# Kernel optimization log

Hardware: AMD Instinct MI355X
Metric: run time of the kernel (lower is better)

Reference implementation:

```python
import jax, jax.numpy as jnp
import numpy as np

D_MODEL = 1024
N_HEADS = 16
HEAD_DIM = D_MODEL // N_HEADS
D_C = 128
THETA = 10000.0


def rope_cos_sin(timestamps):
    # timestamps: (B, L) -> cos, sin: (B, L, HEAD_DIM)
    freqs = 1.0 / (THETA ** (jnp.arange(0, HEAD_DIM, 2, dtype=jnp.float32) / HEAD_DIM))
    t = timestamps[..., None] * freqs            # (B, L, HEAD_DIM//2)
    emb = jnp.concatenate([t, t], axis=-1)       # (B, L, HEAD_DIM)
    return jnp.cos(emb), jnp.sin(emb)


def rotate_half(x):
    x1, x2 = jnp.split(x, 2, axis=-1)
    return jnp.concatenate([-x2, x1], axis=-1)


def setup_inputs() -> dict:
    key = jax.random.key(0)
    ks = jax.random.split(key, 10)
    B, L = 2, 2048
    s = 0.02
    return {
        "query": jax.random.normal(ks[0], (B, L, D_MODEL), jnp.float32),
        "timestamps_q": jax.random.uniform(ks[1], (B, L), jnp.float32) * 365.0,
        "timestamps_kv": jax.random.uniform(ks[2], (B, L), jnp.float32) * 365.0,
        "w_kv_c": jax.random.normal(ks[3], (D_MODEL, D_C), jnp.float32) * s,
        "w_kc_up": jax.random.normal(ks[4], (D_C, D_MODEL), jnp.float32) * s,
        "w_vc_up": jax.random.normal(ks[5], (D_C, D_MODEL), jnp.float32) * s,
        "w_qr": jax.random.normal(ks[6], (D_MODEL, D_MODEL), jnp.float32) * s,
        "w_kr": jax.random.normal(ks[7], (D_MODEL, D_MODEL), jnp.float32) * s,
        "w_o": jax.random.normal(ks[8], (D_MODEL, D_MODEL), jnp.float32) * s,
    }


def reference(query, timestamps_q, timestamps_kv, w_kv_c, w_kc_up, w_vc_up, w_qr, w_kr, w_o):
    B, Lq, _ = query.shape
    key_value = query  # self-attention path (key_value defaults to query)
    Lk = key_value.shape[1]

    def heads(x, L):  # (B, L, D) -> (B, H, L, hd)
        return x.reshape(B, L, N_HEADS, HEAD_DIM).transpose(0, 2, 1, 3)

    c_kv = key_value @ w_kv_c                      # (B, Lk, d_c) low-rank KV
    k_c = heads(c_kv @ w_kc_up, Lk)
    v_c = heads(c_kv @ w_vc_up, Lk)
    q_r = heads(query @ w_qr, Lq)
    k_r = heads(key_value @ w_kr, Lk)

    cos_q, _ = rope_cos_sin(timestamps_q)
    cos_k, _ = rope_cos_sin(timestamps_kv)
    cos_q = cos_q[:, None]                          # (B, 1, Lq, hd)
    cos_k = cos_k[:, None]                          # (B, 1, Lk, hd)
    # Faithful to original (which passes cos_k in the `sin` slot):
    q_r = q_r * cos_q + rotate_half(q_r) * cos_k
    k_r = k_r * cos_q + rotate_half(k_r) * cos_k

    scale = HEAD_DIM ** -0.5
    qs = q_r * scale
    attn = jnp.einsum("bhqd,bhkd->bhqk", qs, k_c) + jnp.einsum("bhqd,bhkd->bhqk", qs, k_r)
    attn_weights = jax.nn.softmax(attn, axis=-1)
    out = jnp.einsum("bhqk,bhkd->bhqd", attn_weights, v_c)
    out = out.transpose(0, 2, 1, 3).reshape(B, Lq, D_MODEL)
    return out @ w_o
```

## Files before the change

kernel.cpp:

```cpp
#include <hip/hip_runtime.h>

typedef float          f32x4    __attribute__((ext_vector_type(4)));
typedef float          float8v  __attribute__((ext_vector_type(8)));
typedef unsigned short ushort8v __attribute__((ext_vector_type(8)));
typedef __bf16         bf16x8   __attribute__((ext_vector_type(8)));
typedef __bf16         bf16x4   __attribute__((ext_vector_type(4)));

__device__ __forceinline__ unsigned short f2b(float x) {
  union { __bf16 b; unsigned short u; } v;
  v.b = (__bf16)x;
  return v.u;
}
__device__ __forceinline__ float b2f(unsigned short h) {
  union { unsigned u; float f; } v; v.u = ((unsigned)h) << 16;
  return v.f;
}
__device__ __forceinline__ void lds_fence() {
  __builtin_amdgcn_wave_barrier();
  asm volatile("s_waitcnt lgkmcnt(0)" ::: "memory");
}

__device__ __forceinline__ void g2lds16(const unsigned short* g,
                                        unsigned short* l) {
  __builtin_amdgcn_global_load_lds(
      (const __attribute__((address_space(1))) unsigned int*)g,
      (__attribute__((address_space(3))) unsigned int*)l, 16, 0, 0);
}

__global__ void cvt_kernel(const float* __restrict__ src,
                           unsigned short* __restrict__ dst, int n8) {
  int i = blockIdx.x * 256 + threadIdx.x;
  if (i >= n8) return;
  float8v v = reinterpret_cast<const float8v*>(src)[i];
  ushort8v h;
#pragma unroll
  for (int j = 0; j < 8; ++j) h[j] = f2b(v[j]);
  reinterpret_cast<ushort8v*>(dst)[i] = h;
}

__global__ __launch_bounds__(256) void wtrans_kernel(
    const float* __restrict__ W, unsigned short* __restrict__ WT,
    int K, int N) {
  __shared__ unsigned short T[64 * 72];
  const int tid = threadIdx.x;
  const int n0 = blockIdx.x * 64, k0 = blockIdx.y * 64;
#pragma unroll
  for (int it = 0; it < 2; ++it) {
    int c = tid + it * 256;
    int r = c >> 3, cc = c & 7;
    float8v v = *reinterpret_cast<const float8v*>(
        &W[(size_t)(k0 + r) * N + n0 + cc * 8]);
    ushort8v h;
#pragma unroll
    for (int j = 0; j < 8; ++j) h[j] = f2b(v[j]);
    *reinterpret_cast<ushort8v*>(&T[r * 72 + cc * 8]) = h;
  }
  __syncthreads();
#pragma unroll
  for (int it = 0; it < 2; ++it) {
    int c = tid + it * 256;
    int n = c >> 3, kc = c & 7;
    ushort8v y;
#pragma unroll
    for (int j = 0; j < 8; ++j) y[j] = T[(kc * 8 + j) * 72 + n];
    *reinterpret_cast<ushort8v*>(&WT[(size_t)(n0 + n) * K + k0 + kc * 8]) = y;
  }
}

template <int TM, typename CT, bool ACC>
__global__ __launch_bounds__(256) void gemm_bt(
    const unsigned short* __restrict__ A, const unsigned short* __restrict__ Bt,
    CT* __restrict__ C, int M, int N, int K) {
  __shared__ unsigned short As[TM * 64];
  __shared__ unsigned short Bs[128 * 64];
  const int tid = threadIdx.x;
  const int m0 = blockIdx.y * TM, n0 = blockIdx.x * 128;
  const int wave = tid >> 6, lane = tid & 63;
  const int wm = (wave >> 1) * (TM / 2), wn = (wave & 1) * 64;
  const int l16 = lane & 15, quad = lane >> 4;
  constexpr int MI = TM / 32;

  f32x4 acc[MI][4];
#pragma unroll
  for (int i = 0; i < MI; ++i)
#pragma unroll
    for (int j = 0; j < 4; ++j)
#pragma unroll
      for (int r = 0; r < 4; ++r) acc[i][j][r] = 0.f;

  for (int k0 = 0; k0 < K; k0 += 64) {
    __syncthreads();
#pragma unroll
    for (int it = 0; it < TM * 8 / 256; ++it) {
      int c = it * 256 + tid;
      int m = c >> 3, kc = (c & 7) ^ (m & 7);
      g2lds16(&A[(size_t)(m0 + m) * K + k0 + kc * 8], &As[c * 8]);
    }
#pragma unroll
    for (int it = 0; it < 4; ++it) {
      int c = it * 256 + tid;
      int n = c >> 3, kc = (c & 7) ^ (n & 7);
      g2lds16(&Bt[(size_t)(n0 + n) * K + k0 + kc * 8], &Bs[c * 8]);
    }
    __syncthreads();

#pragma unroll
    for (int ks = 0; ks < 2; ++ks) {
      bf16x8 af[MI], bfr[4];
#pragma unroll
      for (int mi = 0; mi < MI; ++mi) {
        int m = wm + mi * 16 + l16;
        af[mi] = *reinterpret_cast<const bf16x8*>(
            &As[(m * 8 + ((ks * 4 + quad) ^ (m & 7))) * 8]);
      }
#pragma unroll
      for (int ni = 0; ni < 4; ++ni) {
        int n = wn + ni * 16 + l16;
        bfr[ni] = *reinterpret_cast<const bf16x8*>(
            &Bs[(n * 8 + ((ks * 4 + quad) ^ (n & 7))) * 8]);
      }
#pragma unroll
      for (int mi = 0; mi < MI; ++mi)
#pragma unroll
        for (int ni = 0; ni < 4; ++ni)
          acc[mi][ni] = __builtin_amdgcn_mfma_f32_16x16x32_bf16(
              af[mi], bfr[ni], acc[mi][ni], 0, 0, 0);
    }
  }

#pragma unroll
  for (int mi = 0; mi < MI; ++mi)
#pragma unroll
    for (int ni = 0; ni < 4; ++ni) {
      int row = m0 + wm + mi * 16 + quad * 4;
      int col = n0 + wn + ni * 16 + l16;
#pragma unroll
      for (int r = 0; r < 4; ++r) {
        size_t idx = (size_t)(row + r) * N + col;
        float val = acc[mi][ni][r];
        if constexpr (sizeof(CT) == 2) {
          if constexpr (ACC) val += b2f(C[idx]);
          C[idx] = f2b(val);
        } else {
          if constexpr (ACC) val += C[idx];
          C[idx] = val;
        }
      }
    }
}

__global__ __launch_bounds__(256) void gemm_fused3(
    const unsigned short* __restrict__ A, const unsigned short* __restrict__ Bt,
    unsigned short* __restrict__ Cq, unsigned short* __restrict__ Ck,
    unsigned short* __restrict__ Cc, int K) {
  __shared__ unsigned short As[1024 * 8];
  __shared__ unsigned short Bs[1024 * 8];
  const int tid = threadIdx.x;
  const int m0 = blockIdx.y * 128, n0 = blockIdx.x * 128;
  const int wave = tid >> 6, lane = tid & 63;
  const int wm = (wave >> 1) * 64, wn = (wave & 1) * 64;
  const int l16 = lane & 15, quad = lane >> 4;

  f32x4 acc[4][4];
#pragma unroll
  for (int i = 0; i < 4; ++i)
#pragma unroll
    for (int j = 0; j < 4; ++j)
#pragma unroll
      for (int r = 0; r < 4; ++r) acc[i][j][r] = 0.f;

  for (int k0 = 0; k0 < K; k0 += 64) {
    __syncthreads();
#pragma unroll
    for (int it = 0; it < 4; ++it) {
      int c = it * 256 + tid;
      int m = c >> 3, kc = (c & 7) ^ (m & 7);
      g2lds16(&A[(size_t)(m0 + m) * K + k0 + kc * 8], &As[c * 8]);
    }
#pragma unroll
    for (int it = 0; it < 4; ++it) {
      int c = it * 256 + tid;
      int n = c >> 3, kc = (c & 7) ^ (n & 7);
      g2lds16(&Bt[(size_t)(n0 + n) * K + k0 + kc * 8], &Bs[c * 8]);
    }
    __syncthreads();

#pragma unroll
    for (int ks = 0; ks < 2; ++ks) {
      bf16x8 af[4], bfr[4];
#pragma unroll
      for (int mi = 0; mi < 4; ++mi) {
        int m = wm + mi * 16 + l16;
        af[mi] = *reinterpret_cast<const bf16x8*>(
            &As[(m * 8 + ((ks * 4 + quad) ^ (m & 7))) * 8]);
      }
#pragma unroll
      for (int ni = 0; ni < 4; ++ni) {
        int n = wn + ni * 16 + l16;
        bfr[ni] = *reinterpret_cast<const bf16x8*>(
            &Bs[(n * 8 + ((ks * 4 + quad) ^ (n & 7))) * 8]);
      }
#pragma unroll
      for (int mi = 0; mi < 4; ++mi)
#pragma unroll
        for (int ni = 0; ni < 4; ++ni)
          acc[mi][ni] = __builtin_amdgcn_mfma_f32_16x16x32_bf16(
              af[mi], bfr[ni], acc[mi][ni], 0, 0, 0);
    }
  }

  unsigned short* dst;
  int w, cb;
  if (n0 < 1024)      { dst = Cq; w = 1024; cb = 0; }
  else if (n0 < 2048) { dst = Ck; w = 1024; cb = 1024; }
  else                { dst = Cc; w = 128;  cb = 2048; }
#pragma unroll
  for (int mi = 0; mi < 4; ++mi)
#pragma unroll
    for (int ni = 0; ni < 4; ++ni) {
      int row = m0 + wm + mi * 16 + quad * 4;
      int col = n0 - cb + wn + ni * 16 + l16;
#pragma unroll
      for (int r = 0; r < 4; ++r)
        dst[(size_t)(row + r) * w + col] = f2b(acc[mi][ni][r]);
    }
}

__global__ __launch_bounds__(256) void gemm_fused2(
    const unsigned short* __restrict__ A, const unsigned short* __restrict__ Bt,
    unsigned short* __restrict__ Ck, unsigned short* __restrict__ Cv, int K) {
  __shared__ unsigned short As[1024 * 8];
  __shared__ unsigned short Bs[1024 * 8];
  const int tid = threadIdx.x;
  const int m0 = blockIdx.y * 128, n0 = blockIdx.x * 128;
  const int wave = tid >> 6, lane = tid & 63;
  const int wm = (wave >> 1) * 64, wn = (wave & 1) * 64;
  const int l16 = lane & 15, quad = lane >> 4;

  f32x4 acc[4][4];
#pragma unroll
  for (int i = 0; i < 4; ++i)
#pragma unroll
    for (int j = 0; j < 4; ++j)
#pragma unroll
      for (int r = 0; r < 4; ++r) acc[i][j][r] = 0.f;

  for (int k0 = 0; k0 < K; k0 += 64) {
    __syncthreads();
#pragma unroll
    for (int it = 0; it < 4; ++it) {
      int c = it * 256 + tid;
      int m = c >> 3, kc = (c & 7) ^ (m & 7);
      g2lds16(&A[(size_t)(m0 + m) * K + k0 + kc * 8], &As[c * 8]);
    }
#pragma unroll
    for (int it = 0; it < 4; ++it) {
      int c = it * 256 + tid;
      int n = c >> 3, kc = (c & 7) ^ (n & 7);
      g2lds16(&Bt[(size_t)(n0 + n) * K + k0 + kc * 8], &Bs[c * 8]);
    }
    __syncthreads();

#pragma unroll
    for (int ks = 0; ks < 2; ++ks) {
      bf16x8 af[4], bfr[4];
#pragma unroll
      for (int mi = 0; mi < 4; ++mi) {
        int m = wm + mi * 16 + l16;
        af[mi] = *reinterpret_cast<const bf16x8*>(
            &As[(m * 8 + ((ks * 4 + quad) ^ (m & 7))) * 8]);
      }
#pragma unroll
      for (int ni = 0; ni < 4; ++ni) {
        int n = wn + ni * 16 + l16;
        bfr[ni] = *reinterpret_cast<const bf16x8*>(
            &Bs[(n * 8 + ((ks * 4 + quad) ^ (n & 7))) * 8]);
      }
#pragma unroll
      for (int mi = 0; mi < 4; ++mi)
#pragma unroll
        for (int ni = 0; ni < 4; ++ni)
          acc[mi][ni] = __builtin_amdgcn_mfma_f32_16x16x32_bf16(
              af[mi], bfr[ni], acc[mi][ni], 0, 0, 0);
    }
  }

  const bool first = (n0 < 1024);
  unsigned short* dst = first ? Ck : Cv;
  int cb = first ? 0 : 1024;
#pragma unroll
  for (int mi = 0; mi < 4; ++mi)
#pragma unroll
    for (int ni = 0; ni < 4; ++ni) {
      int row = m0 + wm + mi * 16 + quad * 4;
      int col = n0 - cb + wn + ni * 16 + l16;
#pragma unroll
      for (int r = 0; r < 4; ++r) {
        size_t idx = (size_t)(row + r) * 1024 + col;
        float val = acc[mi][ni][r];
        if (first) val += b2f(dst[idx]);
        dst[idx] = f2b(val);
      }
    }
}

__global__ void rope_kernel(unsigned short* __restrict__ qr,
                            unsigned short* __restrict__ kr,
                            const float* __restrict__ tq,
                            const float* __restrict__ tk) {
  int idx = blockIdx.x * 256 + threadIdx.x;
  int i = idx & 31;
  int mh = idx >> 5;
  int m = mh >> 4;
  float f = exp2f(-(float)i * (13.287712379549449f / 32.f));
  float cq = cosf(tq[m] * f);
  float ck = cosf(tk[m] * f);
  size_t base = (size_t)mh * 64;
  const float qscale = 0.18033688011112042f;
  float q1 = b2f(qr[base + i]), q2 = b2f(qr[base + i + 32]);
  float k1 = b2f(kr[base + i]), k2 = b2f(kr[base + i + 32]);
  qr[base + i]      = f2b((q1 * cq - q2 * ck) * qscale);
  qr[base + i + 32] = f2b((q2 * cq + q1 * ck) * qscale);
  kr[base + i]      = f2b(k1 * cq - k2 * ck);
  kr[base + i + 32] = f2b(k2 * cq + k1 * ck);
}

__global__ __launch_bounds__(256) void vtrans_kernel(
    const unsigned short* __restrict__ v, unsigned short* __restrict__ vt,
    int L) {
  __shared__ unsigned short T[64 * 72];
  const int tid = threadIdx.x;
  const int l0 = blockIdx.x * 64, bh = blockIdx.y;
  const size_t inbase = ((size_t)(bh >> 4) * L) * 1024 + (bh & 15) * 64;
  const size_t outbase = (size_t)bh * 64 * L;
#pragma unroll
  for (int it = 0; it < 2; ++it) {
    int c = tid + it * 256;
    int l = c >> 3, dc = c & 7;
    ushort8v x = *reinterpret_cast<const ushort8v*>(
        &v[inbase + (size_t)(l0 + l) * 1024 + dc * 8]);
    *reinterpret_cast<ushort8v*>(&T[l * 72 + dc * 8]) = x;
  }
  __syncthreads();
#pragma unroll
  for (int it = 0; it < 2; ++it) {
    int c = tid + it * 256;
    int d = c >> 3, lc = c & 7;
    ushort8v y;
#pragma unroll
    for (int j = 0; j < 8; ++j) y[j] = T[(lc * 8 + j) * 72 + d];
    *reinterpret_cast<ushort8v*>(&vt[outbase + (size_t)d * L + l0 + lc * 8]) = y;
  }
}

__global__ __launch_bounds__(256) void flash10_kernel(
    const unsigned short* __restrict__ qs, const unsigned short* __restrict__ ks,
    const unsigned short* __restrict__ vt, unsigned short* __restrict__ o,
    int L) {
  __shared__ unsigned short Ks[2][512 * 8];
  __shared__ unsigned short Vs[2][512 * 8];
  __shared__ unsigned short Ps[4][16 * 64];
  const int tid = threadIdx.x;
  const int wave = tid >> 6, lane = tid & 63;
  const int l16 = lane & 15, quad = lane >> 4;
  const int bh = blockIdx.y;
  const int qb = blockIdx.x * 64 + wave * 16;
  const size_t base = ((size_t)(bh >> 4) * L) * 1024 + (bh & 15) * 64;
  const size_t vtbase = (size_t)bh * 64 * L;

  bf16x8 aq[2];
  {
    size_t qrow = base + (size_t)(qb + l16) * 1024;
    aq[0] = *reinterpret_cast<const bf16x8*>(&qs[qrow + quad * 8]);
    aq[1] = *reinterpret_cast<const bf16x8*>(&qs[qrow + 32 + quad * 8]);
  }

  ushort8v onesu;
#pragma unroll
  for (int j = 0; j < 8; ++j) onesu[j] = 0x3F80;
  bf16x8 ones = *reinterpret_cast<bf16x8*>(&onesu);

  f32x4 oacc[4];
  f32x4 lacc;
#pragma unroll
  for (int r = 0; r < 4; ++r) lacc[r] = 0.f;
#pragma unroll
  for (int nt = 0; nt < 4; ++nt)
#pragma unroll
    for (int r = 0; r < 4; ++r) oacc[nt][r] = 0.f;

  const int T = L / 64;
#pragma unroll
  for (int it = 0; it < 2; ++it) {
    int c = it * 256 + tid;
    int key = c >> 3, dc = (c & 7) ^ (key & 7);
    g2lds16(&ks[base + (size_t)key * 1024 + dc * 8], &Ks[0][c * 8]);
  }
#pragma unroll
  for (int it = 0; it < 2; ++it) {
    int c = it * 256 + tid;
    int d = c >> 3, kc = (c & 7) ^ (d & 7);
    g2lds16(&vt[vtbase + (size_t)d * L + kc * 8], &Vs[0][c * 8]);
  }

  for (int t = 0; t < T; ++t) {
    __syncthreads();
    if (t + 1 < T) {
      int k0 = (t + 1) * 64, nb = (t + 1) & 1;
#pragma unroll
      for (int it = 0; it < 2; ++it) {
        int c = it * 256 + tid;
        int key = c >> 3, dc = (c & 7) ^ (key & 7);
        g2lds16(&ks[base + (size_t)(k0 + key) * 1024 + dc * 8], &Ks[nb][c * 8]);
      }
#pragma unroll
      for (int it = 0; it < 2; ++it) {
        int c = it * 256 + tid;
        int d = c >> 3, kc = (c & 7) ^ (d & 7);
        g2lds16(&vt[vtbase + (size_t)d * L + k0 + kc * 8], &Vs[nb][c * 8]);
      }
    }
    const int cb = t & 1;

    f32x4 st[4];
#pragma unroll
    for (int nt = 0; nt < 4; ++nt) {
      int key = nt * 16 + l16;
      int dc0 = quad ^ (key & 7);
      int dc1 = (4 + quad) ^ (key & 7);
      bf16x8 bk0 = *reinterpret_cast<const bf16x8*>(
          &Ks[cb][(key * 8 + dc0) * 8]);
      bf16x8 bk1 = *reinterpret_cast<const bf16x8*>(
          &Ks[cb][(key * 8 + dc1) * 8]);
      f32x4 z; z[0] = z[1] = z[2] = z[3] = 0.f;
      z = __builtin_amdgcn_mfma_f32_16x16x32_bf16(bk0, aq[0], z, 0, 0, 0);
      z = __builtin_amdgcn_mfma_f32_16x16x32_bf16(bk1, aq[1], z, 0, 0, 0);
      st[nt] = z;
    }

    lds_fence();
#pragma unroll
    for (int nt = 0; nt < 4; ++nt) {
      bf16x4 w;
#pragma unroll
      for (int r = 0; r < 4; ++r)
        w[r] = (__bf16)__builtin_amdgcn_exp2f(st[nt][r]);
      int slot = (nt * 2 + (quad >> 1)) ^ (l16 & 7);
      *reinterpret_cast<bf16x4*>(
          &Ps[wave][l16 * 64 + slot * 8 + (quad & 1) * 4]) = w;
    }
    lds_fence();
    bf16x8 ap[2];
#pragma unroll
    for (int hf = 0; hf < 2; ++hf) {
      int slot = (hf * 4 + quad) ^ (l16 & 7);
      ap[hf] = *reinterpret_cast<const bf16x8*>(
          &Ps[wave][l16 * 64 + slot * 8]);
    }
    lacc = __builtin_amdgcn_mfma_f32_16x16x32_bf16(ap[0], ones, lacc, 0, 0, 0);
    lacc = __builtin_amdgcn_mfma_f32_16x16x32_bf16(ap[1], ones, lacc, 0, 0, 0);

#pragma unroll
    for (int nt = 0; nt < 4; ++nt) {
      int d = nt * 16 + l16;
#pragma unroll
      for (int hf = 0; hf < 2; ++hf) {
        int kc = (hf * 4 + quad) ^ (d & 7);
        bf16x8 bv = *reinterpret_cast<const bf16x8*>(
            &Vs[cb][(d * 8 + kc) * 8]);
        oacc[nt] = __builtin_amdgcn_mfma_f32_16x16x32_bf16(
            ap[hf], bv, oacc[nt], 0, 0, 0);
      }
    }
  }

#pragma unroll
  for (int r = 0; r < 4; ++r) {
    float inv = __builtin_amdgcn_rcpf(lacc[r]);
    int q = qb + quad * 4 + r;
#pragma unroll
    for (int nt = 0; nt < 4; ++nt)
      o[base + (size_t)q * 1024 + nt * 16 + l16] = f2b(oacc[nt][r] * inv);
  }
}

extern "C" void kernel_launch(void* const* d_in, const int* in_sizes, int n_in,
                              void* d_out, int out_size, void* d_ws, size_t ws_size,
                              hipStream_t stream) {
  const float* X    = (const float*)d_in[0];
  const float* tq   = (const float*)d_in[1];
  const float* tk   = (const float*)d_in[2];
  const float* wkvc = (const float*)d_in[3];
  const float* wkc  = (const float*)d_in[4];
  const float* wvc  = (const float*)d_in[5];
  const float* wqr  = (const float*)d_in[6];
  const float* wkr  = (const float*)d_in[7];
  const float* wo   = (const float*)d_in[8];

  const int D = 1024, DC = 128, L = 2048;
  const int M = in_sizes[0] / D;
  const int B = M / L;
  const int NBH = B * 16;
  (void)n_in; (void)out_size; (void)ws_size;

  unsigned short* p = (unsigned short*)d_ws;
  auto take = [&](size_t n) { unsigned short* r = p; p += n; return r; };
  unsigned short* Xb    = take((size_t)M * D);
  unsigned short* qsb   = take((size_t)M * D);
  unsigned short* ksb   = take((size_t)M * D);
  unsigned short* vcb   = take((size_t)M * D);
  unsigned short* ckv   = take((size_t)M * DC);
  unsigned short* Wbig  = take((size_t)(2 * D + DC) * D);
  unsigned short* Wkcvc = take((size_t)(2 * D) * DC);
  unsigned short* WoT   = take((size_t)D * D);
  unsigned short* vtb   = Xb;
  unsigned short* obuf  = vcb;

  cvt_kernel<<<(M * D / 8 + 255) / 256, 256, 0, stream>>>(X, Xb, M * D / 8);
  auto wt = [&](const float* W, unsigned short* WT, int K, int N) {
    dim3 g(N / 64, K / 64);
    wtrans_kernel<<<g, 256, 0, stream>>>(W, WT, K, N);
  };
  wt(wqr,  Wbig,                          D, D);
  wt(wkr,  Wbig + (size_t)D * D,          D, D);
  wt(wkvc, Wbig + (size_t)2 * D * D,      D, DC);
  wt(wkc,  Wkcvc,                         DC, D);
  wt(wvc,  Wkcvc + (size_t)D * DC,        DC, D);
  wt(wo,   WoT,                           D, D);

  {
    dim3 g((2 * D + DC) / 128, M / 128);
    gemm_fused3<<<g, 256, 0, stream>>>(Xb, Wbig, qsb, ksb, ckv, D);
  }
  rope_kernel<<<(M * 512) / 256, 256, 0, stream>>>(qsb, ksb, tq, tk);
  {
    dim3 g(2 * D / 128, M / 128);
    gemm_fused2<<<g, 256, 0, stream>>>(ckv, Wkcvc, ksb, vcb, DC);
  }

  dim3 tg(L / 64, NBH);
  vtrans_kernel<<<tg, 256, 0, stream>>>(vcb, vtb, L);

  dim3 fg(L / 64, NBH);
  flash10_kernel<<<fg, 256, 0, stream>>>(qsb, ksb, vtb, obuf, L);

  {
    dim3 g(D / 128, M / 64);
    gemm_bt<64, float, false><<<g, 256, 0, stream>>>(
        obuf, WoT, (float*)d_out, M, D, D);
  }
}
```

Measured before the change: 234.6 us.

## Keep softmax P in registers by permuting V^T key order to match MFMA layout

The flash kernel no longer round-trips the exponentiated score tile through LDS. The P fragments are built directly from the QK^T accumulator registers. To make that register layout line up with the PV MFMA operand, the V transpose kernel writes keys in a permuted order within each 64-key block. This removes per-iteration LDS writes, reads and two wave fences, at the cost of a more scattered, half-width store pattern in the transpose kernel.

```diff
diff --git a/kernel.cpp b/kernel.cpp
--- a/kernel.cpp
+++ b/kernel.cpp
@@ -3,8 +3,8 @@
 typedef float          f32x4    __attribute__((ext_vector_type(4)));
 typedef float          float8v  __attribute__((ext_vector_type(8)));
 typedef unsigned short ushort8v __attribute__((ext_vector_type(8)));
+typedef unsigned short ushort4v __attribute__((ext_vector_type(4)));
 typedef __bf16         bf16x8   __attribute__((ext_vector_type(8)));
-typedef __bf16         bf16x4   __attribute__((ext_vector_type(4)));
 
 __device__ __forceinline__ unsigned short f2b(float x) {
   union { __bf16 b; unsigned short u; } v;
@@ -14,10 +14,6 @@
 __device__ __forceinline__ float b2f(unsigned short h) {
   union { unsigned u; float f; } v; v.u = ((unsigned)h) << 16;
   return v.f;
-}
-__device__ __forceinline__ void lds_fence() {
-  __builtin_amdgcn_wave_barrier();
-  asm volatile("s_waitcnt lgkmcnt(0)" ::: "memory");
 }
 
 __device__ __forceinline__ void g2lds16(const unsigned short* g,
@@ -346,20 +342,24 @@
   for (int it = 0; it < 2; ++it) {
     int c = tid + it * 256;
     int d = c >> 3, lc = c & 7;
-    ushort8v y;
-#pragma unroll
-    for (int j = 0; j < 8; ++j) y[j] = T[(lc * 8 + j) * 72 + d];
-    *reinterpret_cast<ushort8v*>(&vt[outbase + (size_t)d * L + l0 + lc * 8]) = y;
-  }
-}
-
-__global__ __launch_bounds__(256) void flash10_kernel(
+    ushort4v ylo, yhi;
+#pragma unroll
+    for (int j = 0; j < 4; ++j) ylo[j] = T[(lc * 8 + j) * 72 + d];
+#pragma unroll
+    for (int j = 0; j < 4; ++j) yhi[j] = T[(lc * 8 + 4 + j) * 72 + d];
+    int bs = ((lc >> 2) << 5) | ((lc & 1) << 4) | (((lc >> 1) & 1) << 2);
+    size_t row = outbase + (size_t)d * L + l0;
+    *reinterpret_cast<ushort4v*>(&vt[row + bs]) = ylo;
+    *reinterpret_cast<ushort4v*>(&vt[row + bs + 8]) = yhi;
+  }
+}
+
+__global__ __launch_bounds__(256) void flash13_kernel(
     const unsigned short* __restrict__ qs, const unsigned short* __restrict__ ks,
     const unsigned short* __restrict__ vt, unsigned short* __restrict__ o,
     int L) {
   __shared__ unsigned short Ks[2][512 * 8];
   __shared__ unsigned short Vs[2][512 * 8];
-  __shared__ unsigned short Ps[4][16 * 64];
   const int tid = threadIdx.x;
   const int wave = tid >> 6, lane = tid & 63;
   const int l16 = lane & 15, quad = lane >> 4;
@@ -438,25 +438,16 @@
       st[nt] = z;
     }
 
-    lds_fence();
-#pragma unroll
-    for (int nt = 0; nt < 4; ++nt) {
-      bf16x4 w;
-#pragma unroll
-      for (int r = 0; r < 4; ++r)
-        w[r] = (__bf16)__builtin_amdgcn_exp2f(st[nt][r]);
-      int slot = (nt * 2 + (quad >> 1)) ^ (l16 & 7);
-      *reinterpret_cast<bf16x4*>(
-          &Ps[wave][l16 * 64 + slot * 8 + (quad & 1) * 4]) = w;
-    }
-    lds_fence();
     bf16x8 ap[2];
 #pragma unroll
-    for (int hf = 0; hf < 2; ++hf) {
-      int slot = (hf * 4 + quad) ^ (l16 & 7);
-      ap[hf] = *reinterpret_cast<const bf16x8*>(
-          &Ps[wave][l16 * 64 + slot * 8]);
-    }
+    for (int hf = 0; hf < 2; ++hf)
+#pragma unroll
+      for (int w = 0; w < 4; ++w) {
+        int nt = 2 * hf + (w >> 1), p = w & 1;
+        ap[hf][2 * w]     = (__bf16)__builtin_amdgcn_exp2f(st[nt][2 * p]);
+        ap[hf][2 * w + 1] = (__bf16)__builtin_amdgcn_exp2f(st[nt][2 * p + 1]);
+      }
+
     lacc = __builtin_amdgcn_mfma_f32_16x16x32_bf16(ap[0], ones, lacc, 0, 0, 0);
     lacc = __builtin_amdgcn_mfma_f32_16x16x32_bf16(ap[1], ones, lacc, 0, 0, 0);
 
@@ -542,7 +533,7 @@
   vtrans_kernel<<<tg, 256, 0, stream>>>(vcb, vtb, L);
 
   dim3 fg(L / 64, NBH);
-  flash10_kernel<<<fg, 256, 0, stream>>>(qsb, ksb, vtb, obuf, L);
+  flash13_kernel<<<fg, 256, 0, stream>>>(qsb, ksb, vtb, obuf, L);
 
   {
     dim3 g(D / 128, M / 64);
```

Measured after the change: 233.9 us. Within noise of the previous version (-0.3%).
